# Optimization experiments

Hardware: AMD Instinct MI355X
Metric: run time of the kernel (lower is better)

The kernel has to match this reference:

```python
import jax, jax.numpy as jnp
import numpy as np

N_NODES = 14   # input_size: nodes of the graph
SEQ = 24       # seq_len == GAT in/out feature dim == output_size
GAT_HID = 64
MLP_HID = 64
NEG_SLOPE = 0.2  # PyG GATConv default leaky_relu slope
B = 32768
N_EDGES = 56


def setup_inputs() -> dict:
    key = jax.random.key(0)
    ks = jax.random.split(key, 16)
    def w(k, shape, fan_in):
        return jax.random.normal(k, shape, dtype=jnp.float32) / np.sqrt(fan_in)
    return {
        "x": jax.random.normal(ks[0], (B, SEQ, N_NODES), dtype=jnp.float32),
        "edge_index": jax.random.randint(ks[1], (2, N_EDGES), 0, N_NODES, dtype=jnp.int64),
        # GATConv 1: in=24 -> out=64, heads=1
        "W1": w(ks[2], (SEQ, GAT_HID), SEQ),
        "a_src1": w(ks[3], (GAT_HID,), GAT_HID),
        "a_dst1": w(ks[4], (GAT_HID,), GAT_HID),
        "b1": jnp.zeros((GAT_HID,), dtype=jnp.float32),
        # GATConv 2: in=64 -> out=24, heads=1
        "W2": w(ks[5], (GAT_HID, SEQ), GAT_HID),
        "a_src2": w(ks[6], (SEQ,), SEQ),
        "a_dst2": w(ks[7], (SEQ,), SEQ),
        "b2": jnp.zeros((SEQ,), dtype=jnp.float32),
        # per-node 2-layer MLPs (one Linear(24,64)+ReLU+Linear(64,24) per node)
        "fc1_w": w(ks[8], (N_NODES, SEQ, MLP_HID), SEQ),
        "fc1_b": jnp.zeros((N_NODES, MLP_HID), dtype=jnp.float32),
        "fc2_w": w(ks[9], (N_NODES, MLP_HID, SEQ), MLP_HID),
        "fc2_b": jnp.zeros((N_NODES, SEQ), dtype=jnp.float32),
    }


def _gat_conv(x, src, dst, W, a_s, a_d, b):
    # PyG GATConv, heads=1, concat=False: linear -> edge attention -> edge softmax over dst -> scatter-sum
    h = x @ W                                             # [N, F]
    alpha = jax.nn.leaky_relu(h[src] @ a_s + h[dst] @ a_d, NEG_SLOPE)  # [E]
    m = jax.ops.segment_max(alpha, dst, num_segments=N_NODES)
    e = jnp.exp(alpha - m[dst])
    s = jax.ops.segment_sum(e, dst, num_segments=N_NODES)
    w = e / s[dst]
    return jax.ops.segment_sum(h[src] * w[:, None], dst, num_segments=N_NODES) + b


def reference(x, edge_index, W1, a_src1, a_dst1, b1, W2, a_src2, a_dst2, b2,
              fc1_w, fc1_b, fc2_w, fc2_b):
    ei = edge_index.astype(jnp.int32)
    loops = jnp.arange(N_NODES, dtype=jnp.int32)  # add_self_loops=True (PyG default)
    src = jnp.concatenate([ei[0], loops])
    dst = jnp.concatenate([ei[1], loops])

    def gat(xs):  # xs: [N_NODES, SEQ]
        h = jax.nn.elu(_gat_conv(xs, src, dst, W1, a_src1, a_dst1, b1))
        return _gat_conv(h, src, dst, W2, a_src2, a_dst2, b2)

    # x: [B, SEQ, N_NODES] -> transpose(1,2) -> per-sample GAT, vmapped over batch
    g = jax.vmap(gat)(x.transpose(0, 2, 1))              # [B, N_NODES, SEQ]
    # per-node 2-layer MLP, batched over nodes via einsum
    h = jax.nn.relu(jnp.einsum('bnf,nfh->bnh', g, fc1_w) + fc1_b)
    pred = jnp.einsum('bnh,nho->bno', h, fc2_w) + fc2_b  # [B, N_NODES, SEQ]
    return pred.transpose(1, 0, 2)                       # [N_NODES, B, SEQ]
```

## Files before the change

kernel.cpp:

```cpp
#include <hip/hip_runtime.h>

typedef unsigned int uu32;

#define NN 14
#define FD 24
#define HD 64
#define NE 70
#define BB 32768
#define SPW 4
#define WPB 4
#define K1_BLOCKS (BB / (WPB * SPW))
#define K2_BLOCKS (NN * (BB / 256))
#define HAP 68
#define H2P 28
#define PSZ 224

#define WSYNC() asm volatile("s_waitcnt lgkmcnt(0)" ::: "memory")

__global__ __launch_bounds__(256) void gat_k(
    const float* __restrict__ x, const int* __restrict__ ei,
    const float* __restrict__ W1, const float* __restrict__ as1,
    const float* __restrict__ ad1, const float* __restrict__ b1,
    const float* __restrict__ W2, const float* __restrict__ as2,
    const float* __restrict__ ad2, const float* __restrict__ b2,
    float* __restrict__ Gout) {
    __shared__ __align__(16) float XS[WPB][NN * FD];
    __shared__ __align__(16) float HA[WPB][NN * HAP];
    __shared__ __align__(16) float H2S[WPB][NN * H2P];
    __shared__ __align__(16) float PS[WPB][PSZ];
    __shared__ float sdS[WPB][2 * NN];
    __shared__ float smS[WPB][NN];
    __shared__ __align__(16) float a1S[2 * HD];
    __shared__ __align__(16) float a2S[2 * FD];
    __shared__ int esS[NE], edS[NE];

    const int tid = threadIdx.x;
    const int wv = tid >> 6;
    const int lane = tid & 63;
    float* XSw = XS[wv];
    float* HAw = HA[wv];
    float* H2w = H2S[wv];
    float* Pw = PS[wv];
    float* sdw = sdS[wv];
    float* smw = smS[wv];

    if (tid < 2 * HD) a1S[tid] = (tid < HD) ? as1[tid] : ad1[tid - HD];
    if (tid < 2 * FD) a2S[tid] = (tid < FD) ? as2[tid] : ad2[tid - FD];
    if (tid < 56) {
        int e64 = 1;
        for (int i = 0; i < 8; i++)
            if (ei[2 * i + 1] != 0 || (uu32)ei[2 * i] >= (uu32)NN) e64 = 0;
        esS[tid] = e64 ? ei[2 * tid] : ei[tid];
        edS[tid] = e64 ? ei[112 + 2 * tid] : ei[56 + tid];
    } else if (tid < NE) {
        esS[tid] = tid - 56;
        edS[tid] = tid - 56;
    }

    float w1r[FD];
#pragma unroll
    for (int f = 0; f < FD; f++) w1r[f] = W1[f * HD + lane];
    const float b1r = b1[lane];
    const int f2 = lane % FD;
    const int g2 = lane / FD;
    float w2r[HD];
#pragma unroll
    for (int k = 0; k < HD; k++) w2r[k] = W2[k * FD + f2];
    const float b2r = b2[f2];
    __syncthreads();
    const bool ex = (lane < NE - 64);
    const int s0 = esS[lane], d0 = edS[lane];
    const int s1 = esS[ex ? 64 + lane : 0], d1 = edS[ex ? 64 + lane : 0];

    const int gw = blockIdx.x * WPB + wv;
    for (int t = 0; t < SPW; t++) {
        const size_t b = (size_t)gw * SPW + t;
        const float4* xb4 = (const float4*)(x + b * (NN * FD));
        {
            float4 v = xb4[lane];
            int e = 4 * lane;
            XSw[(e % NN) * FD + (e / NN)] = v.x; e++;
            XSw[(e % NN) * FD + (e / NN)] = v.y; e++;
            XSw[(e % NN) * FD + (e / NN)] = v.z; e++;
            XSw[(e % NN) * FD + (e / NN)] = v.w;
            if (lane < 20) {
                v = xb4[64 + lane];
                e = 256 + 4 * lane;
                XSw[(e % NN) * FD + (e / NN)] = v.x; e++;
                XSw[(e % NN) * FD + (e / NN)] = v.y; e++;
                XSw[(e % NN) * FD + (e / NN)] = v.z; e++;
                XSw[(e % NN) * FD + (e / NN)] = v.w;
            }
        }
        WSYNC();
        float acc[NN];
#pragma unroll
        for (int n = 0; n < NN; n++) acc[n] = 0.0f;
#pragma unroll
        for (int k = 0; k < 6; k++) {
#pragma unroll
            for (int n = 0; n < NN; n++) {
                float4 xv = *(const float4*)&XSw[n * FD + 4 * k];
                acc[n] = fmaf(xv.x, w1r[4 * k + 0], acc[n]);
                acc[n] = fmaf(xv.y, w1r[4 * k + 1], acc[n]);
                acc[n] = fmaf(xv.z, w1r[4 * k + 2], acc[n]);
                acc[n] = fmaf(xv.w, w1r[4 * k + 3], acc[n]);
            }
        }
#pragma unroll
        for (int n = 0; n < NN; n++) HAw[n * HAP + lane] = acc[n];
        WSYNC();
        if (lane < 2 * NN) {
            const int v = (lane >= NN) ? 1 : 0;
            const int n2 = lane - v * NN;
            float s = 0.0f;
#pragma unroll
            for (int k = 0; k < 16; k++) {
                float4 h4 = *(const float4*)&HAw[n2 * HAP + 4 * k];
                float4 a4 = *(const float4*)&a1S[v * HD + 4 * k];
                s = fmaf(h4.x, a4.x, s); s = fmaf(h4.y, a4.y, s);
                s = fmaf(h4.z, a4.z, s); s = fmaf(h4.w, a4.w, s);
            }
            sdw[v * NN + n2] = s;
        }
        if (lane < PSZ / 4)
            *(float4*)&Pw[lane * 4] = make_float4(0.f, 0.f, 0.f, 0.f);
        if (lane < NN) smw[lane] = 0.0f;
        WSYNC();
        {
            float a = sdw[s0] + sdw[NN + d0];
            a = a > 0.0f ? a : 0.2f * a;
            float e0 = __expf(a);
            atomicAdd(&smw[d0], e0);
            atomicAdd(&Pw[d0 * 16 + s0], e0);
            if (ex) {
                a = sdw[s1] + sdw[NN + d1];
                a = a > 0.0f ? a : 0.2f * a;
                float e1 = __expf(a);
                atomicAdd(&smw[d1], e1);
                atomicAdd(&Pw[d1 * 16 + s1], e1);
            }
        }
        WSYNC();
        float acc2[NN];
#pragma unroll
        for (int n = 0; n < NN; n++) {
            float a = 0.0f;
#pragma unroll
            for (int k4 = 0; k4 < 3; k4++) {
                float4 p4 = *(const float4*)&Pw[n * 16 + 4 * k4];
                a = fmaf(p4.x, acc[4 * k4 + 0], a);
                a = fmaf(p4.y, acc[4 * k4 + 1], a);
                a = fmaf(p4.z, acc[4 * k4 + 2], a);
                a = fmaf(p4.w, acc[4 * k4 + 3], a);
            }
            float4 p4 = *(const float4*)&Pw[n * 16 + 12];
            a = fmaf(p4.x, acc[12], a);
            a = fmaf(p4.y, acc[13], a);
            a = __fdividef(a, smw[n]) + b1r;
            acc2[n] = a > 0.0f ? a : (__expf(a) - 1.0f);
        }
#pragma unroll
        for (int n = 0; n < NN; n++) HAw[n * HAP + lane] = acc2[n];
        WSYNC();
        if (g2 < 2) {
#pragma unroll
            for (int i = 0; i < 7; i++) {
                const int n = g2 + 2 * i;
                float a = 0.0f;
#pragma unroll
                for (int k4 = 0; k4 < 16; k4++) {
                    float4 v4 = *(const float4*)&HAw[n * HAP + 4 * k4];
                    a = fmaf(v4.x, w2r[4 * k4 + 0], a);
                    a = fmaf(v4.y, w2r[4 * k4 + 1], a);
                    a = fmaf(v4.z, w2r[4 * k4 + 2], a);
                    a = fmaf(v4.w, w2r[4 * k4 + 3], a);
                }
                H2w[n * H2P + f2] = a;
            }
        }
        WSYNC();
        if (lane < 2 * NN) {
            const int v = (lane >= NN) ? 1 : 0;
            const int n2 = lane - v * NN;
            float s = 0.0f;
#pragma unroll
            for (int q = 0; q < 6; q++) {
                float4 h4 = *(const float4*)&H2w[n2 * H2P + 4 * q];
                float4 a4 = *(const float4*)&a2S[v * FD + 4 * q];
                s = fmaf(h4.x, a4.x, s); s = fmaf(h4.y, a4.y, s);
                s = fmaf(h4.z, a4.z, s); s = fmaf(h4.w, a4.w, s);
            }
            sdw[v * NN + n2] = s;
        }
        if (lane < PSZ / 4)
            *(float4*)&Pw[lane * 4] = make_float4(0.f, 0.f, 0.f, 0.f);
        if (lane < NN) smw[lane] = 0.0f;
        WSYNC();
        {
            float a = sdw[s0] + sdw[NN + d0];
            a = a > 0.0f ? a : 0.2f * a;
            float e0 = __expf(a);
            atomicAdd(&smw[d0], e0);
            atomicAdd(&Pw[d0 * 16 + s0], e0);
            if (ex) {
                a = sdw[s1] + sdw[NN + d1];
                a = a > 0.0f ? a : 0.2f * a;
                float e1 = __expf(a);
                atomicAdd(&smw[d1], e1);
                atomicAdd(&Pw[d1 * 16 + s1], e1);
            }
        }
        WSYNC();
        if (g2 < 2) {
            float h2c[NN];
#pragma unroll
            for (int k = 0; k < NN; k++) h2c[k] = H2w[k * H2P + f2];
#pragma unroll
            for (int i = 0; i < 7; i++) {
                const int n = g2 + 2 * i;
                float a = 0.0f;
#pragma unroll
                for (int k4 = 0; k4 < 3; k4++) {
                    float4 p4 = *(const float4*)&Pw[n * 16 + 4 * k4];
                    a = fmaf(p4.x, h2c[4 * k4 + 0], a);
                    a = fmaf(p4.y, h2c[4 * k4 + 1], a);
                    a = fmaf(p4.z, h2c[4 * k4 + 2], a);
                    a = fmaf(p4.w, h2c[4 * k4 + 3], a);
                }
                float4 p4 = *(const float4*)&Pw[n * 16 + 12];
                a = fmaf(p4.x, h2c[12], a);
                a = fmaf(p4.y, h2c[13], a);
                Gout[((size_t)n * BB + b) * FD + f2] =
                    __fdividef(a, smw[n]) + b2r;
            }
        }
        WSYNC();
    }
}

__global__ __launch_bounds__(256) void mlp_k(
    const float* __restrict__ fc1w, const float* __restrict__ fc1b,
    const float* __restrict__ fc2w, const float* __restrict__ fc2b,
    float* __restrict__ gio) {
    const int t = threadIdx.x;
    const int n = blockIdx.x >> 7;
    const int b0 = (blockIdx.x & 127) * 256;

    const float* __restrict__ W1 = fc1w + (size_t)n * (FD * HD);
    const float* __restrict__ W2 = fc2w + (size_t)n * (HD * FD);
    const float* __restrict__ B1 = fc1b + n * HD;
    const float* __restrict__ B2 = fc2b + n * FD;

    const size_t base = ((size_t)n * BB + b0 + t) * FD;
    float g[FD], o[FD];
#pragma unroll
    for (int q = 0; q < 6; q++)
        *(float4*)&g[4 * q] = *(const float4*)&gio[base + 4 * q];
#pragma unroll
    for (int f = 0; f < FD; f++) o[f] = B2[f];

#pragma unroll 1
    for (int j4 = 0; j4 < 16; j4++) {
        float h0 = B1[4 * j4 + 0], h1 = B1[4 * j4 + 1];
        float h2 = B1[4 * j4 + 2], h3 = B1[4 * j4 + 3];
#pragma unroll
        for (int f = 0; f < FD; f++) {
            float4 w4 = *(const float4*)&W1[f * HD + 4 * j4];
            h0 = fmaf(g[f], w4.x, h0);
            h1 = fmaf(g[f], w4.y, h1);
            h2 = fmaf(g[f], w4.z, h2);
            h3 = fmaf(g[f], w4.w, h3);
        }
        h0 = fmaxf(h0, 0.f); h1 = fmaxf(h1, 0.f);
        h2 = fmaxf(h2, 0.f); h3 = fmaxf(h3, 0.f);
        float hv[4] = {h0, h1, h2, h3};
#pragma unroll
        for (int u2 = 0; u2 < 4; u2++) {
            const int j = 4 * j4 + u2;
#pragma unroll
            for (int f4 = 0; f4 < 6; f4++) {
                float4 w4 = *(const float4*)&W2[j * FD + 4 * f4];
                o[4 * f4 + 0] = fmaf(hv[u2], w4.x, o[4 * f4 + 0]);
                o[4 * f4 + 1] = fmaf(hv[u2], w4.y, o[4 * f4 + 1]);
                o[4 * f4 + 2] = fmaf(hv[u2], w4.z, o[4 * f4 + 2]);
                o[4 * f4 + 3] = fmaf(hv[u2], w4.w, o[4 * f4 + 3]);
            }
        }
    }
#pragma unroll
    for (int q = 0; q < 6; q++)
        *(float4*)&gio[base + 4 * q] = *(const float4*)&o[4 * q];
}

extern "C" void kernel_launch(void* const* d_in, const int* in_sizes, int n_in,
                              void* d_out, int out_size, void* d_ws, size_t ws_size,
                              hipStream_t stream) {
    (void)in_sizes; (void)n_in; (void)out_size; (void)d_ws; (void)ws_size;
    const float* x    = (const float*)d_in[0];
    const int*   ei   = (const int*)d_in[1];
    const float* W1   = (const float*)d_in[2];
    const float* as1  = (const float*)d_in[3];
    const float* ad1  = (const float*)d_in[4];
    const float* b1   = (const float*)d_in[5];
    const float* W2   = (const float*)d_in[6];
    const float* as2  = (const float*)d_in[7];
    const float* ad2  = (const float*)d_in[8];
    const float* b2   = (const float*)d_in[9];
    const float* fc1w = (const float*)d_in[10];
    const float* fc1b = (const float*)d_in[11];
    const float* fc2w = (const float*)d_in[12];
    const float* fc2b = (const float*)d_in[13];
    float* gio = (float*)d_out;

    gat_k<<<dim3(K1_BLOCKS), dim3(256), 0, stream>>>(
        x, ei, W1, as1, ad1, b1, W2, as2, ad2, b2, gio);
    mlp_k<<<dim3(K2_BLOCKS), dim3(256), 0, stream>>>(
        fc1w, fc1b, fc2w, fc2b, gio);
}
```

Measured before the change: 351.7 us.

## Read GAT input directly via scalar loads; stage MLP weights in LDS, two rows per thread

The GAT kernel drops its LDS transpose staging of x. It reads each sample through a wave-uniform pointer set with readfirstlane, so the compiler can use scalar loads broadcast to all lanes. The MLP kernel now copies each node's fc weights and biases into shared memory and processes two batch rows per thread, halving the block count. This reuses each weight load across two rows, at the cost of higher register pressure and possibly lower occupancy.

```diff
diff --git a/kernel.cpp b/kernel.cpp
--- a/kernel.cpp
+++ b/kernel.cpp
@@ -10,7 +10,8 @@
 #define SPW 4
 #define WPB 4
 #define K1_BLOCKS (BB / (WPB * SPW))
-#define K2_BLOCKS (NN * (BB / 256))
+#define R2 2
+#define K2_BLOCKS (NN * (BB / (256 * R2)))
 #define HAP 68
 #define H2P 28
 #define PSZ 224
@@ -24,7 +25,6 @@
     const float* __restrict__ W2, const float* __restrict__ as2,
     const float* __restrict__ ad2, const float* __restrict__ b2,
     float* __restrict__ Gout) {
-    __shared__ __align__(16) float XS[WPB][NN * FD];
     __shared__ __align__(16) float HA[WPB][NN * HAP];
     __shared__ __align__(16) float H2S[WPB][NN * H2P];
     __shared__ __align__(16) float PS[WPB][PSZ];
@@ -37,7 +37,6 @@
     const int tid = threadIdx.x;
     const int wv = tid >> 6;
     const int lane = tid & 63;
-    float* XSw = XS[wv];
     float* HAw = HA[wv];
     float* H2w = H2S[wv];
     float* Pw = PS[wv];
@@ -74,38 +73,18 @@
 
     const int gw = blockIdx.x * WPB + wv;
     for (int t = 0; t < SPW; t++) {
-        const size_t b = (size_t)gw * SPW + t;
-        const float4* xb4 = (const float4*)(x + b * (NN * FD));
-        {
-            float4 v = xb4[lane];
-            int e = 4 * lane;
-            XSw[(e % NN) * FD + (e / NN)] = v.x; e++;
-            XSw[(e % NN) * FD + (e / NN)] = v.y; e++;
-            XSw[(e % NN) * FD + (e / NN)] = v.z; e++;
-            XSw[(e % NN) * FD + (e / NN)] = v.w;
-            if (lane < 20) {
-                v = xb4[64 + lane];
-                e = 256 + 4 * lane;
-                XSw[(e % NN) * FD + (e / NN)] = v.x; e++;
-                XSw[(e % NN) * FD + (e / NN)] = v.y; e++;
-                XSw[(e % NN) * FD + (e / NN)] = v.z; e++;
-                XSw[(e % NN) * FD + (e / NN)] = v.w;
-            }
-        }
-        WSYNC();
+        const int b = gw * SPW + t;
+        const int bo = __builtin_amdgcn_readfirstlane(b * (NN * FD));
+        const float* __restrict__ xb = x + bo;
         float acc[NN];
 #pragma unroll
         for (int n = 0; n < NN; n++) acc[n] = 0.0f;
 #pragma unroll
-        for (int k = 0; k < 6; k++) {
-#pragma unroll
-            for (int n = 0; n < NN; n++) {
-                float4 xv = *(const float4*)&XSw[n * FD + 4 * k];
-                acc[n] = fmaf(xv.x, w1r[4 * k + 0], acc[n]);
-                acc[n] = fmaf(xv.y, w1r[4 * k + 1], acc[n]);
-                acc[n] = fmaf(xv.z, w1r[4 * k + 2], acc[n]);
-                acc[n] = fmaf(xv.w, w1r[4 * k + 3], acc[n]);
-            }
+        for (int f = 0; f < FD; f++) {
+            const float wf = w1r[f];
+#pragma unroll
+            for (int n = 0; n < NN; n++)
+                acc[n] = fmaf(xb[f * NN + n], wf, acc[n]);
         }
 #pragma unroll
         for (int n = 0; n < NN; n++) HAw[n * HAP + lane] = acc[n];
@@ -243,54 +222,77 @@
     const float* __restrict__ fc1w, const float* __restrict__ fc1b,
     const float* __restrict__ fc2w, const float* __restrict__ fc2b,
     float* __restrict__ gio) {
+    __shared__ __align__(16) float W1L[FD * HD];
+    __shared__ __align__(16) float W2L[HD * FD];
+    __shared__ float B1L[HD];
+    __shared__ float B2L[FD];
+
     const int t = threadIdx.x;
-    const int n = blockIdx.x >> 7;
-    const int b0 = (blockIdx.x & 127) * 256;
-
-    const float* __restrict__ W1 = fc1w + (size_t)n * (FD * HD);
-    const float* __restrict__ W2 = fc2w + (size_t)n * (HD * FD);
-    const float* __restrict__ B1 = fc1b + n * HD;
-    const float* __restrict__ B2 = fc2b + n * FD;
-
-    const size_t base = ((size_t)n * BB + b0 + t) * FD;
-    float g[FD], o[FD];
-#pragma unroll
-    for (int q = 0; q < 6; q++)
-        *(float4*)&g[4 * q] = *(const float4*)&gio[base + 4 * q];
-#pragma unroll
-    for (int f = 0; f < FD; f++) o[f] = B2[f];
+    const int n = blockIdx.x >> 6;
+    const int b0 = (blockIdx.x & 63) * 512;
+
+    const float4* w1p = (const float4*)(fc1w + (size_t)n * (FD * HD));
+    const float4* w2p = (const float4*)(fc2w + (size_t)n * (HD * FD));
+    for (int i = t; i < 384; i += 256) {
+        *(float4*)&W1L[4 * i] = w1p[i];
+        *(float4*)&W2L[4 * i] = w2p[i];
+    }
+    if (t < HD) B1L[t] = fc1b[n * HD + t];
+    if (t < FD) B2L[t] = fc2b[n * FD + t];
+    __syncthreads();
+
+    const size_t base0 = ((size_t)n * BB + b0 + t) * FD;
+    const size_t base1 = base0 + (size_t)256 * FD;
+    float g0[FD], g1[FD], o0[FD], o1[FD];
+#pragma unroll
+    for (int q = 0; q < 6; q++) {
+        *(float4*)&g0[4 * q] = *(const float4*)&gio[base0 + 4 * q];
+        *(float4*)&g1[4 * q] = *(const float4*)&gio[base1 + 4 * q];
+    }
+#pragma unroll
+    for (int f = 0; f < FD; f++) { o0[f] = B2L[f]; o1[f] = o0[f]; }
 
 #pragma unroll 1
     for (int j4 = 0; j4 < 16; j4++) {
-        float h0 = B1[4 * j4 + 0], h1 = B1[4 * j4 + 1];
-        float h2 = B1[4 * j4 + 2], h3 = B1[4 * j4 + 3];
+        float h00 = B1L[4 * j4 + 0], h01 = B1L[4 * j4 + 1];
+        float h02 = B1L[4 * j4 + 2], h03 = B1L[4 * j4 + 3];
+        float h10 = h00, h11 = h01, h12 = h02, h13 = h03;
 #pragma unroll
         for (int f = 0; f < FD; f++) {
-            float4 w4 = *(const float4*)&W1[f * HD + 4 * j4];
-            h0 = fmaf(g[f], w4.x, h0);
-            h1 = fmaf(g[f], w4.y, h1);
-            h2 = fmaf(g[f], w4.z, h2);
-            h3 = fmaf(g[f], w4.w, h3);
-        }
-        h0 = fmaxf(h0, 0.f); h1 = fmaxf(h1, 0.f);
-        h2 = fmaxf(h2, 0.f); h3 = fmaxf(h3, 0.f);
-        float hv[4] = {h0, h1, h2, h3};
+            float4 w4 = *(const float4*)&W1L[f * HD + 4 * j4];
+            h00 = fmaf(g0[f], w4.x, h00); h01 = fmaf(g0[f], w4.y, h01);
+            h02 = fmaf(g0[f], w4.z, h02); h03 = fmaf(g0[f], w4.w, h03);
+            h10 = fmaf(g1[f], w4.x, h10); h11 = fmaf(g1[f], w4.y, h11);
+            h12 = fmaf(g1[f], w4.z, h12); h13 = fmaf(g1[f], w4.w, h13);
+        }
+        h00 = fmaxf(h00, 0.f); h01 = fmaxf(h01, 0.f);
+        h02 = fmaxf(h02, 0.f); h03 = fmaxf(h03, 0.f);
+        h10 = fmaxf(h10, 0.f); h11 = fmaxf(h11, 0.f);
+        h12 = fmaxf(h12, 0.f); h13 = fmaxf(h13, 0.f);
+        float hv0[4] = {h00, h01, h02, h03};
+        float hv1[4] = {h10, h11, h12, h13};
 #pragma unroll
         for (int u2 = 0; u2 < 4; u2++) {
             const int j = 4 * j4 + u2;
 #pragma unroll
             for (int f4 = 0; f4 < 6; f4++) {
-                float4 w4 = *(const float4*)&W2[j * FD + 4 * f4];
-                o[4 * f4 + 0] = fmaf(hv[u2], w4.x, o[4 * f4 + 0]);
-                o[4 * f4 + 1] = fmaf(hv[u2], w4.y, o[4 * f4 + 1]);
-                o[4 * f4 + 2] = fmaf(hv[u2], w4.z, o[4 * f4 + 2]);
-                o[4 * f4 + 3] = fmaf(hv[u2], w4.w, o[4 * f4 + 3]);
-            }
-        }
-    }
-#pragma unroll
-    for (int q = 0; q < 6; q++)
-        *(float4*)&gio[base + 4 * q] = *(const float4*)&o[4 * q];
+                float4 w4 = *(const float4*)&W2L[j * FD + 4 * f4];
+                o0[4 * f4 + 0] = fmaf(hv0[u2], w4.x, o0[4 * f4 + 0]);
+                o0[4 * f4 + 1] = fmaf(hv0[u2], w4.y, o0[4 * f4 + 1]);
+                o0[4 * f4 + 2] = fmaf(hv0[u2], w4.z, o0[4 * f4 + 2]);
+                o0[4 * f4 + 3] = fmaf(hv0[u2], w4.w, o0[4 * f4 + 3]);
+                o1[4 * f4 + 0] = fmaf(hv1[u2], w4.x, o1[4 * f4 + 0]);
+                o1[4 * f4 + 1] = fmaf(hv1[u2], w4.y, o1[4 * f4 + 1]);
+                o1[4 * f4 + 2] = fmaf(hv1[u2], w4.z, o1[4 * f4 + 2]);
+                o1[4 * f4 + 3] = fmaf(hv1[u2], w4.w, o1[4 * f4 + 3]);
+            }
+        }
+    }
+#pragma unroll
+    for (int q = 0; q < 6; q++) {
+        *(float4*)&gio[base0 + 4 * q] = *(const float4*)&o0[4 * q];
+        *(float4*)&gio[base1 + 4 * q] = *(const float4*)&o1[4 * q];
+    }
 }
 
 extern "C" void kernel_launch(void* const* d_in, const int* in_sizes, int n_in,
```

Measured after the change: 369.2 us. 1.05x slower.
